# Kernel optimization log

Hardware: AMD Instinct MI355X
Metric: run time of the kernel (lower is better)

## Reference

```python
import jax, jax.numpy as jnp
import numpy as np

H = 16  # num_heads
EPS = 1e-5


def _ln(x, g, b):
    m = x.mean(-1, keepdims=True)
    v = x.var(-1, keepdims=True)
    return (x - m) / jnp.sqrt(v + EPS) * g + b


def _heads(x):
    b, s, d = x.shape
    return x.reshape(b, s, H, d // H).transpose(0, 2, 1, 3)  # [B,H,S,dh]


def _merge_buggy(z):
    # replicate torch view([B,H,S,dh] -> [B,S,H*dh]) WITHOUT head transpose
    b, h, s, dh = z.shape
    return z.reshape(b, s, h * dh)


def _attn(q_in, kv_in, resid, wq, bq, wk, bk, wv, bv, g, be, scale_by_seq, apply_triu):
    q = _heads(q_in @ wq + bq)
    k = _heads(kv_in @ wk + bk)
    v = _heads(kv_in @ wv + bv)
    qk = jnp.einsum('bhqd,bhkd->bhqk', q, k)
    qk = jnp.where(jnp.isnan(qk), -jnp.inf, qk)
    if scale_by_seq:
        qk = qk / jnp.sqrt(jnp.asarray(qk.shape[-1], qk.dtype))  # sqrt(seq_len), as in source
    a = jax.nn.softmax(qk, axis=-1)
    a = jnp.where(jnp.isnan(a), 0.0, a)
    v = jnp.where(jnp.isnan(v), 0.0, v)
    if apply_triu:
        s = a.shape[-1]
        a = a * jnp.triu(jnp.ones((s, s), a.dtype))  # post-softmax multiplicative mask
    z = jnp.einsum('bhqk,bhkd->bhqd', a, v)
    z = _merge_buggy(z)
    return _ln(resid + z, g, be)


def setup_inputs() -> dict:
    key = jax.random.key(0)
    ks = jax.random.split(key, 20)
    B, S, D, F = 2, 2048, 1024, 1024
    p = lambda k, sh: (jax.random.normal(k, sh, jnp.float32) * 0.02)
    inp = {
        'encoded': jax.random.normal(ks[0], (B, S, D), jnp.float32),
        'decoded': jax.random.normal(ks[1], (B, S, D), jnp.float32),
        'sa_wq': p(ks[2], (D, D)), 'sa_bq': jnp.zeros((D,), jnp.float32),
        'sa_wk': p(ks[3], (D, D)), 'sa_bk': jnp.zeros((D,), jnp.float32),
        'sa_wv': p(ks[4], (D, D)), 'sa_bv': jnp.zeros((D,), jnp.float32),
        'sa_g': jnp.ones((D,), jnp.float32), 'sa_b': jnp.zeros((D,), jnp.float32),
        'ca_wq': p(ks[5], (D, D)), 'ca_bq': jnp.zeros((D,), jnp.float32),
        'ca_wk': p(ks[6], (D, D)), 'ca_bk': jnp.zeros((D,), jnp.float32),
        'ca_wv': p(ks[7], (D, D)), 'ca_bv': jnp.zeros((D,), jnp.float32),
        'ca_g': jnp.ones((D,), jnp.float32), 'ca_b': jnp.zeros((D,), jnp.float32),
        'ffn_w1': p(ks[8], (D, F)), 'ffn_b1': jnp.zeros((F,), jnp.float32),
        'ffn_w2': p(ks[9], (F, D)), 'ffn_b2': jnp.zeros((D,), jnp.float32),
        'ffn_g': jnp.ones((D,), jnp.float32), 'ffn_b': jnp.zeros((D,), jnp.float32),
    }
    return inp


def reference(encoded, decoded,
              sa_wq, sa_bq, sa_wk, sa_bk, sa_wv, sa_bv, sa_g, sa_b,
              ca_wq, ca_bq, ca_wk, ca_bk, ca_wv, ca_bv, ca_g, ca_b,
              ffn_w1, ffn_b1, ffn_w2, ffn_b2, ffn_g, ffn_b):
    # masked self-attention (quirky: scale by sqrt(S), post-softmax triu mask)
    x = _attn(decoded, decoded, decoded, sa_wq, sa_bq, sa_wk, sa_bk, sa_wv, sa_bv,
              sa_g, sa_b, scale_by_seq=True, apply_triu=True)
    # cross-attention (no scale, no mask)
    x = _attn(x, encoded, x, ca_wq, ca_bq, ca_wk, ca_bk, ca_wv, ca_bv,
              ca_g, ca_b, scale_by_seq=False, apply_triu=False)
    # FFN with residual + LayerNorm (dropout = identity in eval)
    y = jax.nn.relu(x @ ffn_w1 + ffn_b1) @ ffn_w2 + ffn_b2
    return _ln(y + x, ffn_g, ffn_b)
```

## Files before the change

kernel.cpp:

```cpp
#include <hip/hip_runtime.h>
#include <hip/hip_bf16.h>
#include <cstdint>


typedef __attribute__((ext_vector_type(8))) short bf16x8;
typedef __attribute__((ext_vector_type(4))) float f32x4;
typedef unsigned short u16;

#define MFMA16(a, b, c) __builtin_amdgcn_mfma_f32_16x16x32_bf16((a), (b), (c), 0, 0, 0)

__device__ __forceinline__ u16 f2b(float f) {
    __hip_bfloat16 h = __float2bfloat16(f);
    return __builtin_bit_cast(u16, h);
}
__device__ __forceinline__ float b2f(u16 u) {
    return __builtin_bit_cast(float, (uint32_t)u << 16);
}
__device__ __forceinline__ void g2lds16(const u16* g, u16* l) {
    __builtin_amdgcn_global_load_lds((const __attribute__((address_space(1))) void*)g,
                                     (__attribute__((address_space(3))) void*)l, 16, 0, 0);
}

__global__ __launch_bounds__(256) void cast_bf16_kernel(const float* __restrict__ x,
                                                        u16* __restrict__ y, int n4) {
    int i = blockIdx.x * 256 + threadIdx.x;
    if (i >= n4) return;
    float4 v = reinterpret_cast<const float4*>(x)[i];
    ushort4 o;
    o.x = f2b(v.x); o.y = f2b(v.y); o.z = f2b(v.z); o.w = f2b(v.w);
    reinterpret_cast<ushort4*>(y)[i] = o;
}

__global__ __launch_bounds__(256) void wcast_all_kernel(
    const float* __restrict__ w0, const float* __restrict__ w1,
    const float* __restrict__ w2, const float* __restrict__ w3,
    const float* __restrict__ w4, const float* __restrict__ w5,
    const float* __restrict__ w6, const float* __restrict__ w7,
    u16* __restrict__ wt) {
    __shared__ float t[32][33];
    const float* W;
    switch (blockIdx.z) {
        case 0: W = w0; break; case 1: W = w1; break;
        case 2: W = w2; break; case 3: W = w3; break;
        case 4: W = w4; break; case 5: W = w5; break;
        case 6: W = w6; break; default: W = w7; break;
    }
    u16* Wt = wt + (size_t)blockIdx.z * 1048576;
    int tx = threadIdx.x & 31, ty = threadIdx.x >> 5;
    int bx = blockIdx.x * 32, by = blockIdx.y * 32;
#pragma unroll
    for (int j = 0; j < 4; ++j)
        t[ty + j * 8][tx] = W[(size_t)(by + ty + j * 8) * 1024 + bx + tx];
    __syncthreads();
#pragma unroll
    for (int j = 0; j < 4; ++j)
        Wt[(size_t)(bx + ty + j * 8) * 1024 + by + tx] = f2b(t[tx][ty + j * 8]);
}

__global__ __launch_bounds__(256) void vtrans_kernel(const u16* __restrict__ V,
                                                     u16* __restrict__ Vt) {
    __shared__ u16 t[32][34];
    const int tx = threadIdx.x & 31, ty = threadIdx.x >> 5;
    const int s0 = blockIdx.x * 32, d0 = blockIdx.y * 32, b = blockIdx.z;
    const u16* src = V + (size_t)b * 2048 * 1024;
    u16* dst = Vt + (size_t)b * 1024 * 2048;
#pragma unroll
    for (int j = 0; j < 4; ++j)
        t[ty + j * 8][tx] = src[(size_t)(s0 + ty + j * 8) * 1024 + d0 + tx];
    __syncthreads();
#pragma unroll
    for (int j = 0; j < 4; ++j)
        dst[(size_t)(d0 + ty + j * 8) * 2048 + s0 + tx] = t[tx][ty + j * 8];
}

__global__ __launch_bounds__(256) void gemm_kernel(
    const u16* __restrict__ A0, const u16* __restrict__ A1,
    const u16* __restrict__ Btb,
    const float* __restrict__ bias0, const float* __restrict__ bias1,
    const float* __restrict__ bias2,
    u16* __restrict__ o0, u16* __restrict__ o1, u16* __restrict__ o2,
    int relu, float oscale0) {
    const int K = 1024;
    __shared__ __align__(16) u16 As[2][128][32];
    __shared__ __align__(16) u16 Bs[2][128][32];
    const int tid = threadIdx.x, lane = tid & 63, w = tid >> 6;
    const int wm = w >> 1, wn = w & 1, l15 = lane & 15, l4 = lane >> 4;
    const int nx = gridDim.x;
    const int fhw = blockIdx.y * nx + blockIdx.x;
    const int cpx = (nx * 32) >> 3;
    const int lid = (fhw & 7) * cpx + (fhw >> 3);
    const int bm = (lid & 31) * 128, bn = (lid >> 5) * 128;
    const int which = bn >> 10;
    const u16* A = (which == 0) ? A0 : A1;
    const int srow = lane >> 2, sc = lane & 3;
    const int scs = (sc ^ (srow & 3)) * 8;
    const u16* aW = A + (size_t)(bm + w * 16 + srow) * K + scs;
    const u16* bW = Btb + (size_t)(bn + w * 16 + srow) * K + scs;
    f32x4 acc[4][4] = {};

#define GSTAGE(bf, kt)                                                  \
    do {                                                                \
        g2lds16(aW + (kt), &As[bf][w * 16][0]);                         \
        g2lds16(aW + (size_t)64 * K + (kt), &As[bf][64 + w * 16][0]);   \
        g2lds16(bW + (kt), &Bs[bf][w * 16][0]);                         \
        g2lds16(bW + (size_t)64 * K + (kt), &Bs[bf][64 + w * 16][0]);   \
    } while (0)

    const int nt = K / 32;
    GSTAGE(0, 0);
    for (int t = 0; t < nt; ++t) {
        __syncthreads();
        if (t + 1 < nt) GSTAGE((t + 1) & 1, (t + 1) * 32);
        const int bf = t & 1;
        bf16x8 af[4], bfr[4];
#pragma unroll
        for (int m = 0; m < 4; ++m) {
            int row = wm * 64 + m * 16 + l15;
            af[m] = *reinterpret_cast<const bf16x8*>(&As[bf][row][(l4 ^ (l15 & 3)) * 8]);
        }
#pragma unroll
        for (int n = 0; n < 4; ++n) {
            int row = wn * 64 + n * 16 + l15;
            bfr[n] = *reinterpret_cast<const bf16x8*>(&Bs[bf][row][(l4 ^ (l15 & 3)) * 8]);
        }
        __builtin_amdgcn_s_setprio(1);
#pragma unroll
        for (int m = 0; m < 4; ++m)
#pragma unroll
            for (int n = 0; n < 4; ++n)
                acc[m][n] = MFMA16(af[m], bfr[n], acc[m][n]);
        __builtin_amdgcn_s_setprio(0);
    }
#undef GSTAGE
    const float* bias = which == 0 ? bias0 : (which == 1 ? bias1 : bias2);
    u16* outp = which == 0 ? o0 : (which == 1 ? o1 : o2);
    const float osc = which == 0 ? oscale0 : 1.0f;
    const int bnl = bn & 1023;
#pragma unroll
    for (int m = 0; m < 4; ++m) {
#pragma unroll
        for (int n = 0; n < 4; ++n) {
            int col = bnl + wn * 64 + n * 16 + l15;
            float bv = bias[col];
            int row0 = bm + wm * 64 + m * 16 + l4 * 4;
#pragma unroll
            for (int r = 0; r < 4; ++r) {
                float v = (acc[m][n][r] + bv) * osc;
                if (relu) v = fmaxf(v, 0.f);
                outp[(size_t)(row0 + r) * 1024 + col] = f2b(v);
            }
        }
    }
}

__global__ __launch_bounds__(256) void gemm64_kernel(
    const u16* __restrict__ A, const u16* __restrict__ Btb,
    const float* __restrict__ bias, u16* __restrict__ outp, int relu) {
    const int K = 1024;
    __shared__ __align__(16) u16 As[2][64][32];
    __shared__ __align__(16) u16 Bs[2][128][32];
    const int tid = threadIdx.x, lane = tid & 63, w = tid >> 6;
    const int wm = w >> 1, wn = w & 1, l15 = lane & 15, l4 = lane >> 4;
    const int fhw = blockIdx.y * 8 + blockIdx.x;
    const int lid = (fhw & 7) * 64 + (fhw >> 3);
    const int bm = (lid & 63) * 64, bn = (lid >> 6) * 128;
    const int srow = lane >> 2, sc = lane & 3;
    const int scs = (sc ^ (srow & 3)) * 8;
    const u16* aW = A + (size_t)(bm + w * 16 + srow) * K + scs;
    const u16* bW = Btb + (size_t)(bn + w * 16 + srow) * K + scs;
    f32x4 acc[2][4] = {};

#define GSTAGE64(bf, kt)                                                \
    do {                                                                \
        g2lds16(aW + (kt), &As[bf][w * 16][0]);                         \
        g2lds16(bW + (kt), &Bs[bf][w * 16][0]);                         \
        g2lds16(bW + (size_t)64 * K + (kt), &Bs[bf][64 + w * 16][0]);   \
    } while (0)

    const int nt = K / 32;
    GSTAGE64(0, 0);
    for (int t = 0; t < nt; ++t) {
        __syncthreads();
        if (t + 1 < nt) GSTAGE64((t + 1) & 1, (t + 1) * 32);
        const int bf = t & 1;
        bf16x8 af[2], bfr[4];
#pragma unroll
        for (int m = 0; m < 2; ++m) {
            int row = wm * 32 + m * 16 + l15;
            af[m] = *reinterpret_cast<const bf16x8*>(&As[bf][row][(l4 ^ (l15 & 3)) * 8]);
        }
#pragma unroll
        for (int n = 0; n < 4; ++n) {
            int row = wn * 64 + n * 16 + l15;
            bfr[n] = *reinterpret_cast<const bf16x8*>(&Bs[bf][row][(l4 ^ (l15 & 3)) * 8]);
        }
        __builtin_amdgcn_s_setprio(1);
#pragma unroll
        for (int m = 0; m < 2; ++m)
#pragma unroll
            for (int n = 0; n < 4; ++n)
                acc[m][n] = MFMA16(af[m], bfr[n], acc[m][n]);
        __builtin_amdgcn_s_setprio(0);
    }
#undef GSTAGE64
#pragma unroll
    for (int m = 0; m < 2; ++m) {
#pragma unroll
        for (int n = 0; n < 4; ++n) {
            int col = bn + wn * 64 + n * 16 + l15;
            float bv = bias[col];
            int row0 = bm + wm * 32 + m * 16 + l4 * 4;
#pragma unroll
            for (int r = 0; r < 4; ++r) {
                float v = acc[m][n][r] + bv;
                if (relu) v = fmaxf(v, 0.f);
                outp[(size_t)(row0 + r) * 1024 + col] = f2b(v);
            }
        }
    }
}

template <int CAUSAL>
__global__ __launch_bounds__(256) void attn_kernel(const u16* __restrict__ Qb,
                                                   const u16* __restrict__ Kb,
                                                   const u16* __restrict__ Vt,
                                                   u16* __restrict__ Z) {
    const int S = 2048, D = 1024;
    __shared__ __align__(16) u16 Ks[2][64][64];
    __shared__ __align__(16) u16 Vs[2][64][64];
    __shared__ __align__(16) u16 Ps[4][16][64];
    const int tid = threadIdx.x, lane = tid & 63, w = tid >> 6;
    const int l15 = lane & 15, l4 = lane >> 4;
    const int hwid = blockIdx.x;
    const int wkid = (hwid & 7) * 128 + (hwid >> 3);
    const int qb = wkid & 31, h = (wkid >> 5) & 15, b = wkid >> 9;
    const int q0 = qb * 64 + w * 16;
    const int qg = q0 + l15;
    const size_t baseQ = (size_t)b * S * D + h * 64;
    const size_t baseVt = ((size_t)(b * 16 + h) * 64) * 2048;

    bf16x8 aq0, aq1;
    {
        const u16* qp = Qb + baseQ + (size_t)qg * D + l4 * 8;
        aq0 = *reinterpret_cast<const bf16x8*>(qp);
        aq1 = *reinterpret_cast<const bf16x8*>(qp + 32);
    }
    float lrp0 = 0.f, lrp1 = 0.f, lrp2 = 0.f, lrp3 = 0.f;
    f32x4 Oacc[4] = {};

    const int swzA = (l4 ^ (l15 & 7)) * 8;
    const int swzB = ((l4 + 4) ^ (l15 & 7)) * 8;
    const u16* ksbA = &Ks[0][l15][swzA];
    const u16* ksbB = &Ks[0][l15][swzB];
    const u16* vsbA = &Vs[0][l15][swzA];
    const u16* vsbB = &Vs[0][l15][swzB];
    const int px = l15 & 7;
    u16* pswp[4];
#pragma unroll
    for (int kg = 0; kg < 4; ++kg)
        pswp[kg] = &Ps[w][l15][((2 * kg + (l4 >> 1)) ^ px) * 8 + (l4 & 1) * 4];
    const u16* psrp0 = &Ps[w][l15][((4 * 0 + l4) ^ px) * 8];
    const u16* psrp1 = &Ps[w][l15][((4 * 1 + l4) ^ px) * 8];

    const int srow = lane >> 3, sc8 = lane & 7;
    const int scs = (sc8 ^ srow) * 8;
    const u16* kWn0 = Kb + baseQ + (size_t)(srow + (w * 2 + 0) * 8) * D + scs;
    const u16* kWn1 = Kb + baseQ + (size_t)(srow + (w * 2 + 1) * 8) * D + scs;
    const u16* vWn0 = Vt + baseVt + (size_t)(srow + (w * 2 + 0) * 8) * 2048 + scs;
    const u16* vWn1 = Vt + baseVt + (size_t)(srow + (w * 2 + 1) * 8) * 2048 + scs;

    const int NT = S / 64;
    const int t0pv = CAUSAL ? qb : 0;

    g2lds16(kWn0, &Ks[0][(w * 2 + 0) * 8][0]);
    g2lds16(kWn1, &Ks[0][(w * 2 + 1) * 8][0]);
    kWn0 += 64 * D; kWn1 += 64 * D;
    if (0 >= t0pv) {
        g2lds16(vWn0, &Vs[0][(w * 2 + 0) * 8][0]);
        g2lds16(vWn1, &Vs[0][(w * 2 + 1) * 8][0]);
    }
    vWn0 += 64; vWn1 += 64;

    int tcur = 0;
#define ATILE(B)                                                               \
    do {                                                                       \
        __syncthreads();                                                       \
        if (tcur + 1 < NT) {                                                   \
            g2lds16(kWn0, &Ks[(B) ^ 1][(w * 2 + 0) * 8][0]);                   \
            g2lds16(kWn1, &Ks[(B) ^ 1][(w * 2 + 1) * 8][0]);                   \
            if (tcur + 1 >= t0pv) {                                            \
                g2lds16(vWn0, &Vs[(B) ^ 1][(w * 2 + 0) * 8][0]);               \
                g2lds16(vWn1, &Vs[(B) ^ 1][(w * 2 + 1) * 8][0]);               \
            }                                                                  \
        }                                                                      \
        kWn0 += 64 * D; kWn1 += 64 * D; vWn0 += 64; vWn1 += 64;                \
        const bool dopv = (tcur >= t0pv);                                      \
        const bool maskT = CAUSAL && (tcur == qb);                             \
        bf16x8 vf[2][4];                                                       \
        if (dopv) {                                                            \
            _Pragma("unroll")                                                  \
            for (int n = 0; n < 4; ++n) {                                      \
                vf[0][n] = *reinterpret_cast<const bf16x8*>(                   \
                    vsbA + (B) * 4096 + n * 1024);                             \
                vf[1][n] = *reinterpret_cast<const bf16x8*>(                   \
                    vsbB + (B) * 4096 + n * 1024);                             \
            }                                                                  \
        }                                                                      \
        const f32x4 zero = {0.f, 0.f, 0.f, 0.f};                               \
        _Pragma("unroll")                                                      \
        for (int kg = 0; kg < 4; ++kg) {                                       \
            bf16x8 k0 = *reinterpret_cast<const bf16x8*>(                      \
                ksbA + (B) * 4096 + kg * 1024);                                \
            bf16x8 k1 = *reinterpret_cast<const bf16x8*>(                      \
                ksbB + (B) * 4096 + kg * 1024);                                \
            f32x4 sv = MFMA16(k0, aq0, zero);                                  \
            sv = MFMA16(k1, aq1, sv);                                          \
            float e0 = __builtin_exp2f(sv[0]);                                 \
            float e1 = __builtin_exp2f(sv[1]);                                 \
            float e2 = __builtin_exp2f(sv[2]);                                 \
            float e3 = __builtin_exp2f(sv[3]);                                 \
            lrp0 += e0; lrp1 += e1; lrp2 += e2; lrp3 += e3;                    \
            if (dopv) {                                                        \
                if (maskT) {                                                   \
                    int key = tcur * 64 + kg * 16 + l4 * 4;                    \
                    if (key + 0 < qg) e0 = 0.f;                                \
                    if (key + 1 < qg) e1 = 0.f;                                \
                    if (key + 2 < qg) e2 = 0.f;                                \
                    if (key + 3 < qg) e3 = 0.f;                                \
                }                                                              \
                ushort4 pw;                                                    \
                pw.x = f2b(e0); pw.y = f2b(e1);                                \
                pw.z = f2b(e2); pw.w = f2b(e3);                                \
                *reinterpret_cast<ushort4*>(pswp[kg]) = pw;                    \
            }                                                                  \
        }                                                                      \
        if (dopv) {                                                            \
            asm volatile("s_waitcnt lgkmcnt(0)" ::: "memory");                 \
            __builtin_amdgcn_sched_barrier(0);                                 \
            __builtin_amdgcn_s_setprio(1);                                     \
            bf16x8 pa0 = *reinterpret_cast<const bf16x8*>(psrp0);              \
            bf16x8 pa1 = *reinterpret_cast<const bf16x8*>(psrp1);              \
            _Pragma("unroll")                                                  \
            for (int n = 0; n < 4; ++n)                                        \
                Oacc[n] = MFMA16(vf[0][n], pa0, Oacc[n]);                      \
            _Pragma("unroll")                                                  \
            for (int n = 0; n < 4; ++n)                                        \
                Oacc[n] = MFMA16(vf[1][n], pa1, Oacc[n]);                      \
            __builtin_amdgcn_s_setprio(0);                                     \
        }                                                                      \
        ++tcur;                                                                \
    } while (0)

    for (int i = 0; i < NT / 2; ++i) {
        ATILE(0);
        ATILE(1);
    }
#undef ATILE

    float lr = (lrp0 + lrp1) + (lrp2 + lrp3);
    lr += __shfl_xor(lr, 16);
    lr += __shfl_xor(lr, 32);

    {
        float inv = 1.f / lr;
        int orow = h * 128 + (qg >> 4);
        int oc0 = (qg & 15) * 64;
#pragma unroll
        for (int n = 0; n < 4; ++n) {
            ushort4 o;
            o.x = f2b(Oacc[n][0] * inv); o.y = f2b(Oacc[n][1] * inv);
            o.z = f2b(Oacc[n][2] * inv); o.w = f2b(Oacc[n][3] * inv);
            *reinterpret_cast<ushort4*>(
                &Z[(size_t)b * S * D + (size_t)orow * D + oc0 + n * 16 + l4 * 4]) = o;
        }
    }
}

__global__ __launch_bounds__(256) void add_ln_kernel(const float* __restrict__ resid,
                                                     const u16* __restrict__ zb,
                                                     const float* __restrict__ g,
                                                     const float* __restrict__ bb,
                                                     float* __restrict__ outF,
                                                     u16* __restrict__ outH) {
    const int row = blockIdx.x * 4 + (threadIdx.x >> 6);
    const int lane = threadIdx.x & 63;
    const float* rp = resid + (size_t)row * 1024;
    const u16* zp = zb + (size_t)row * 1024;
    float v[16];
    float s = 0.f, s2 = 0.f;
#pragma unroll
    for (int k = 0; k < 4; ++k) {
        int col = k * 256 + lane * 4;
        float4 rv = *reinterpret_cast<const float4*>(rp + col);
        ushort4 zv = *reinterpret_cast<const ushort4*>(zp + col);
        float x0 = rv.x + b2f(zv.x);
        float x1 = rv.y + b2f(zv.y);
        float x2 = rv.z + b2f(zv.z);
        float x3 = rv.w + b2f(zv.w);
        v[k * 4 + 0] = x0; v[k * 4 + 1] = x1; v[k * 4 + 2] = x2; v[k * 4 + 3] = x3;
        s += x0 + x1 + x2 + x3;
        s2 += x0 * x0 + x1 * x1 + x2 * x2 + x3 * x3;
    }
#pragma unroll
    for (int o = 32; o >= 1; o >>= 1) {
        s += __shfl_xor(s, o);
        s2 += __shfl_xor(s2, o);
    }
    float mean = s * (1.f / 1024.f);
    float var = s2 * (1.f / 1024.f) - mean * mean;
    float rstd = rsqrtf(var + 1e-5f);
#pragma unroll
    for (int k = 0; k < 4; ++k) {
        int col = k * 256 + lane * 4;
        float4 gv = *reinterpret_cast<const float4*>(g + col);
        float4 bv = *reinterpret_cast<const float4*>(bb + col);
        float o0 = (v[k * 4 + 0] - mean) * rstd * gv.x + bv.x;
        float o1 = (v[k * 4 + 1] - mean) * rstd * gv.y + bv.y;
        float o2 = (v[k * 4 + 2] - mean) * rstd * gv.z + bv.z;
        float o3 = (v[k * 4 + 3] - mean) * rstd * gv.w + bv.w;
        if (outF) {
            float4 o = make_float4(o0, o1, o2, o3);
            *reinterpret_cast<float4*>(outF + (size_t)row * 1024 + col) = o;
        }
        if (outH) {
            ushort4 o;
            o.x = f2b(o0); o.y = f2b(o1); o.z = f2b(o2); o.w = f2b(o3);
            *reinterpret_cast<ushort4*>(outH + (size_t)row * 1024 + col) = o;
        }
    }
}

extern "C" void kernel_launch(void* const* d_in, const int* in_sizes, int n_in,
                              void* d_out, int out_size, void* d_ws, size_t ws_size,
                              hipStream_t stream) {
    const float* enc   = (const float*)d_in[0];
    const float* dec   = (const float*)d_in[1];
    const float* sa_wq = (const float*)d_in[2];  const float* sa_bq = (const float*)d_in[3];
    const float* sa_wk = (const float*)d_in[4];  const float* sa_bk = (const float*)d_in[5];
    const float* sa_wv = (const float*)d_in[6];  const float* sa_bv = (const float*)d_in[7];
    const float* sa_g  = (const float*)d_in[8];  const float* sa_b  = (const float*)d_in[9];
    const float* ca_wq = (const float*)d_in[10]; const float* ca_bq = (const float*)d_in[11];
    const float* ca_wk = (const float*)d_in[12]; const float* ca_bk = (const float*)d_in[13];
    const float* ca_wv = (const float*)d_in[14]; const float* ca_bv = (const float*)d_in[15];
    const float* ca_g  = (const float*)d_in[16]; const float* ca_b  = (const float*)d_in[17];
    const float* w1    = (const float*)d_in[18]; const float* b1    = (const float*)d_in[19];
    const float* w2    = (const float*)d_in[20]; const float* b2    = (const float*)d_in[21];
    const float* fg    = (const float*)d_in[22]; const float* fb    = (const float*)d_in[23];
    float* out = (float*)d_out;

    const size_t WSZ = 1048576;
    const size_t ASZ = 4194304;

    u16* wt   = (u16*)d_ws;
    u16* decB = wt + 8 * WSZ;
    u16* encB = decB + ASZ;
    u16* qB   = encB + ASZ;
    u16* kB   = qB + ASZ;
    u16* vB   = kB + ASZ;
    u16* zB   = vB + ASZ;
    float* x1f = (float*)(zB + ASZ);
    u16* xb   = (u16*)(x1f + ASZ);

    const float Q_SCALE_SELF = 0.031879354f;
    const float Q_SCALE_CROSS = 1.4426950408889634f;

    wcast_all_kernel<<<dim3(32, 32, 8), 256, 0, stream>>>(sa_wq, sa_wk, sa_wv, ca_wq,
                                                          ca_wk, ca_wv, w1, w2, wt);
    cast_bf16_kernel<<<4096, 256, 0, stream>>>(dec, decB, (int)(ASZ / 4));
    cast_bf16_kernel<<<4096, 256, 0, stream>>>(enc, encB, (int)(ASZ / 4));

    gemm_kernel<<<dim3(24, 32), 256, 0, stream>>>(decB, decB, wt,
                                                  sa_bq, sa_bk, sa_bv, qB, kB, vB,
                                                  0, Q_SCALE_SELF);
    vtrans_kernel<<<dim3(64, 32, 2), 256, 0, stream>>>(vB, xb);
    attn_kernel<1><<<1024, 256, 0, stream>>>(qB, kB, xb, zB);
    add_ln_kernel<<<1024, 256, 0, stream>>>(dec, zB, sa_g, sa_b, x1f, xb);

    gemm_kernel<<<dim3(24, 32), 256, 0, stream>>>(xb, encB, wt + 3 * WSZ,
                                                  ca_bq, ca_bk, ca_bv, qB, kB, vB,
                                                  0, Q_SCALE_CROSS);
    vtrans_kernel<<<dim3(64, 32, 2), 256, 0, stream>>>(vB, xb);
    attn_kernel<0><<<1024, 256, 0, stream>>>(qB, kB, xb, zB);
    add_ln_kernel<<<1024, 256, 0, stream>>>(x1f, zB, ca_g, ca_b, x1f, xb);

    gemm64_kernel<<<dim3(8, 64), 256, 0, stream>>>(xb, wt + 6 * WSZ, b1, qB, 1);
    gemm64_kernel<<<dim3(8, 64), 256, 0, stream>>>(qB, wt + 7 * WSZ, b2, zB, 0);
    add_ln_kernel<<<1024, 256, 0, stream>>>(x1f, zB, fg, fb, out, nullptr);
}
```

Baseline: 330.8 us.

## Triple-buffer attention K/V tiles with 32-key steps and vmcnt-based waits

The attention kernel now walks keys in 32-wide tiles with a three-stage LDS ring for K and V. It waits on vmcnt counts plus a raw s_barrier instead of a full __syncthreads, so loads two tiles ahead can stay in flight while the current tile is computed. The LDS footprint shrinks and the loop is fully unrolled over 64 tiles. In exchange, each tile carries more barrier overhead relative to its compute. V is now loaded for every tile, including causal tiles that get skipped, and the padded P buffer drops its swizzle, which may bring bank conflicts.

```diff
diff --git a/kernel.cpp b/kernel.cpp
--- a/kernel.cpp
+++ b/kernel.cpp
@@ -226,9 +226,9 @@
                                                    const u16* __restrict__ Vt,
                                                    u16* __restrict__ Z) {
     const int S = 2048, D = 1024;
-    __shared__ __align__(16) u16 Ks[2][64][64];
-    __shared__ __align__(16) u16 Vs[2][64][64];
-    __shared__ __align__(16) u16 Ps[4][16][64];
+    __shared__ __align__(16) u16 Ks[3][32][64];
+    __shared__ __align__(16) u16 Vs[3][64][32];
+    __shared__ __align__(16) u16 Ps[4][16][40];
     const int tid = threadIdx.x, lane = tid & 63, w = tid >> 6;
     const int l15 = lane & 15, l4 = lane >> 4;
     const int hwid = blockIdx.x;
@@ -248,71 +248,52 @@
     float lrp0 = 0.f, lrp1 = 0.f, lrp2 = 0.f, lrp3 = 0.f;
     f32x4 Oacc[4] = {};
 
-    const int swzA = (l4 ^ (l15 & 7)) * 8;
-    const int swzB = ((l4 + 4) ^ (l15 & 7)) * 8;
-    const u16* ksbA = &Ks[0][l15][swzA];
-    const u16* ksbB = &Ks[0][l15][swzB];
-    const u16* vsbA = &Vs[0][l15][swzA];
-    const u16* vsbB = &Vs[0][l15][swzB];
-    const int px = l15 & 7;
-    u16* pswp[4];
-#pragma unroll
-    for (int kg = 0; kg < 4; ++kg)
-        pswp[kg] = &Ps[w][l15][((2 * kg + (l4 >> 1)) ^ px) * 8 + (l4 & 1) * 4];
-    const u16* psrp0 = &Ps[w][l15][((4 * 0 + l4) ^ px) * 8];
-    const u16* psrp1 = &Ps[w][l15][((4 * 1 + l4) ^ px) * 8];
-
-    const int srow = lane >> 3, sc8 = lane & 7;
-    const int scs = (sc8 ^ srow) * 8;
-    const u16* kWn0 = Kb + baseQ + (size_t)(srow + (w * 2 + 0) * 8) * D + scs;
-    const u16* kWn1 = Kb + baseQ + (size_t)(srow + (w * 2 + 1) * 8) * D + scs;
-    const u16* vWn0 = Vt + baseVt + (size_t)(srow + (w * 2 + 0) * 8) * 2048 + scs;
-    const u16* vWn1 = Vt + baseVt + (size_t)(srow + (w * 2 + 1) * 8) * 2048 + scs;
-
-    const int NT = S / 64;
-    const int t0pv = CAUSAL ? qb : 0;
-
-    g2lds16(kWn0, &Ks[0][(w * 2 + 0) * 8][0]);
-    g2lds16(kWn1, &Ks[0][(w * 2 + 1) * 8][0]);
-    kWn0 += 64 * D; kWn1 += 64 * D;
-    if (0 >= t0pv) {
-        g2lds16(vWn0, &Vs[0][(w * 2 + 0) * 8][0]);
-        g2lds16(vWn1, &Vs[0][(w * 2 + 1) * 8][0]);
-    }
-    vWn0 += 64; vWn1 += 64;
+    const u16* ksbA = &Ks[0][l15][(l4 ^ (l15 & 7)) * 8];
+    const u16* ksbB = &Ks[0][l15][((l4 + 4) ^ (l15 & 7)) * 8];
+    const u16* vsb  = &Vs[0][l15][(l4 ^ (l15 & 3)) * 8];
+    u16* pswb = &Ps[w][l15][l4 * 4];
+    const u16* psrb = &Ps[w][l15][l4 * 8];
+
+    const u16* kWn = Kb + baseQ + (size_t)(w * 8 + (lane >> 3)) * D +
+                     ((lane & 7) ^ (lane >> 3)) * 8;
+    const u16* vWn = Vt + baseVt + (size_t)(w * 16 + (lane >> 2)) * 2048 +
+                     (((lane & 3) ^ ((lane >> 2) & 3)) * 8);
+
+    const int t0pv = CAUSAL ? (2 * qb) : 0;
+
+    g2lds16(kWn, &Ks[0][w * 8][0]);
+    g2lds16(vWn, &Vs[0][w * 16][0]);
+    kWn += 32 * D; vWn += 32;
+    g2lds16(kWn, &Ks[1][w * 8][0]);
+    g2lds16(vWn, &Vs[1][w * 16][0]);
+    kWn += 32 * D; vWn += 32;
 
     int tcur = 0;
-#define ATILE(B)                                                               \
+#define ATILE(B, VCSTR, DOSTAGE)                                               \
     do {                                                                       \
-        __syncthreads();                                                       \
-        if (tcur + 1 < NT) {                                                   \
-            g2lds16(kWn0, &Ks[(B) ^ 1][(w * 2 + 0) * 8][0]);                   \
-            g2lds16(kWn1, &Ks[(B) ^ 1][(w * 2 + 1) * 8][0]);                   \
-            if (tcur + 1 >= t0pv) {                                            \
-                g2lds16(vWn0, &Vs[(B) ^ 1][(w * 2 + 0) * 8][0]);               \
-                g2lds16(vWn1, &Vs[(B) ^ 1][(w * 2 + 1) * 8][0]);               \
-            }                                                                  \
+        asm volatile("s_waitcnt " VCSTR ::: "memory");                         \
+        __builtin_amdgcn_s_barrier();                                          \
+        if (DOSTAGE) {                                                         \
+            g2lds16(kWn, &Ks[((B) + 2) % 3][w * 8][0]);                        \
+            g2lds16(vWn, &Vs[((B) + 2) % 3][w * 16][0]);                       \
         }                                                                      \
-        kWn0 += 64 * D; kWn1 += 64 * D; vWn0 += 64; vWn1 += 64;                \
-        const bool dopv = (tcur >= t0pv);                                      \
-        const bool maskT = CAUSAL && (tcur == qb);                             \
-        bf16x8 vf[2][4];                                                       \
+        kWn += 32 * D; vWn += 32;                                              \
+        const bool dopv = (!CAUSAL) || (tcur >= t0pv);                         \
+        const bool maskT = CAUSAL && dopv && (tcur * 32 < q0 + 16);            \
+        bf16x8 vf[4];                                                          \
         if (dopv) {                                                            \
             _Pragma("unroll")                                                  \
-            for (int n = 0; n < 4; ++n) {                                      \
-                vf[0][n] = *reinterpret_cast<const bf16x8*>(                   \
-                    vsbA + (B) * 4096 + n * 1024);                             \
-                vf[1][n] = *reinterpret_cast<const bf16x8*>(                   \
-                    vsbB + (B) * 4096 + n * 1024);                             \
-            }                                                                  \
+            for (int n = 0; n < 4; ++n)                                        \
+                vf[n] = *reinterpret_cast<const bf16x8*>(                      \
+                    vsb + (B) * 2048 + n * 512);                               \
         }                                                                      \
         const f32x4 zero = {0.f, 0.f, 0.f, 0.f};                               \
         _Pragma("unroll")                                                      \
-        for (int kg = 0; kg < 4; ++kg) {                                       \
+        for (int kg = 0; kg < 2; ++kg) {                                       \
             bf16x8 k0 = *reinterpret_cast<const bf16x8*>(                      \
-                ksbA + (B) * 4096 + kg * 1024);                                \
+                ksbA + (B) * 2048 + kg * 1024);                                \
             bf16x8 k1 = *reinterpret_cast<const bf16x8*>(                      \
-                ksbB + (B) * 4096 + kg * 1024);                                \
+                ksbB + (B) * 2048 + kg * 1024);                                \
             f32x4 sv = MFMA16(k0, aq0, zero);                                  \
             sv = MFMA16(k1, aq1, sv);                                          \
             float e0 = __builtin_exp2f(sv[0]);                                 \
@@ -322,7 +303,7 @@
             lrp0 += e0; lrp1 += e1; lrp2 += e2; lrp3 += e3;                    \
             if (dopv) {                                                        \
                 if (maskT) {                                                   \
-                    int key = tcur * 64 + kg * 16 + l4 * 4;                    \
+                    int key = tcur * 32 + kg * 16 + l4 * 4;                    \
                     if (key + 0 < qg) e0 = 0.f;                                \
                     if (key + 1 < qg) e1 = 0.f;                                \
                     if (key + 2 < qg) e2 = 0.f;                                \
@@ -331,30 +312,31 @@
                 ushort4 pw;                                                    \
                 pw.x = f2b(e0); pw.y = f2b(e1);                                \
                 pw.z = f2b(e2); pw.w = f2b(e3);                                \
-                *reinterpret_cast<ushort4*>(pswp[kg]) = pw;                    \
+                *reinterpret_cast<ushort4*>(pswb + kg * 16) = pw;              \
             }                                                                  \
         }                                                                      \
         if (dopv) {                                                            \
             asm volatile("s_waitcnt lgkmcnt(0)" ::: "memory");                 \
             __builtin_amdgcn_sched_barrier(0);                                 \
+            bf16x8 pa = *reinterpret_cast<const bf16x8*>(psrb);                \
             __builtin_amdgcn_s_setprio(1);                                     \
-            bf16x8 pa0 = *reinterpret_cast<const bf16x8*>(psrp0);              \
-            bf16x8 pa1 = *reinterpret_cast<const bf16x8*>(psrp1);              \
             _Pragma("unroll")                                                  \
             for (int n = 0; n < 4; ++n)                                        \
-                Oacc[n] = MFMA16(vf[0][n], pa0, Oacc[n]);                      \
-            _Pragma("unroll")                                                  \
-            for (int n = 0; n < 4; ++n)                                        \
-                Oacc[n] = MFMA16(vf[1][n], pa1, Oacc[n]);                      \
+                Oacc[n] = MFMA16(vf[n], pa, Oacc[n]);                          \
             __builtin_amdgcn_s_setprio(0);                                     \
         }                                                                      \
         ++tcur;                                                                \
     } while (0)
 
-    for (int i = 0; i < NT / 2; ++i) {
-        ATILE(0);
-        ATILE(1);
-    }
+    for (int i = 0; i < 20; ++i) {
+        ATILE(0, "vmcnt(2)", true);
+        ATILE(1, "vmcnt(2)", true);
+        ATILE(2, "vmcnt(2)", true);
+    }
+    ATILE(0, "vmcnt(2)", true);
+    ATILE(1, "vmcnt(2)", true);
+    ATILE(2, "vmcnt(2)", false);
+    ATILE(0, "vmcnt(0)", false);
 #undef ATILE
 
     float lr = (lrp0 + lrp1) + (lrp2 + lrp3);
```

Measured after the change: 343.7 us. 3.9% more time.

## Double attention query tile to 128 rows with 8 waves sharing K/V tiles

Applied to the files above, without the earlier changes.

Each attention workgroup now covers 128 query rows with 8 waves (512 threads) instead of 64 rows with 4 waves. Every K/V tile loaded into LDS is reused by twice as many queries, which halves global K/V traffic, and each wave issues one async LDS copy per tile instead of two. The causal path computes a per-wave diagonal tile so the PV skip and masking stay correct. In exchange there are half as many workgroups, larger barriers over 8 waves, and a coarser causal imbalance, where the first four waves of a block do extra V loads they may not need.

```diff
diff --git a/kernel.cpp b/kernel.cpp
--- a/kernel.cpp
+++ b/kernel.cpp
@@ -221,20 +221,20 @@
 }
 
 template <int CAUSAL>
-__global__ __launch_bounds__(256) void attn_kernel(const u16* __restrict__ Qb,
-                                                   const u16* __restrict__ Kb,
-                                                   const u16* __restrict__ Vt,
-                                                   u16* __restrict__ Z) {
+__global__ __launch_bounds__(512, 6) void attn_kernel(const u16* __restrict__ Qb,
+                                                      const u16* __restrict__ Kb,
+                                                      const u16* __restrict__ Vt,
+                                                      u16* __restrict__ Z) {
     const int S = 2048, D = 1024;
     __shared__ __align__(16) u16 Ks[2][64][64];
     __shared__ __align__(16) u16 Vs[2][64][64];
-    __shared__ __align__(16) u16 Ps[4][16][64];
+    __shared__ __align__(16) u16 Ps[8][16][64];
     const int tid = threadIdx.x, lane = tid & 63, w = tid >> 6;
     const int l15 = lane & 15, l4 = lane >> 4;
     const int hwid = blockIdx.x;
-    const int wkid = (hwid & 7) * 128 + (hwid >> 3);
-    const int qb = wkid & 31, h = (wkid >> 5) & 15, b = wkid >> 9;
-    const int q0 = qb * 64 + w * 16;
+    const int wkid = (hwid & 7) * 64 + (hwid >> 3);
+    const int qb = wkid & 15, h = (wkid >> 4) & 15, b = wkid >> 8;
+    const int q0 = qb * 128 + w * 16;
     const int qg = q0 + l15;
     const size_t baseQ = (size_t)b * S * D + h * 64;
     const size_t baseVt = ((size_t)(b * 16 + h) * 64) * 2048;
@@ -262,40 +262,31 @@
     const u16* psrp0 = &Ps[w][l15][((4 * 0 + l4) ^ px) * 8];
     const u16* psrp1 = &Ps[w][l15][((4 * 1 + l4) ^ px) * 8];
 
-    const int srow = lane >> 3, sc8 = lane & 7;
-    const int scs = (sc8 ^ srow) * 8;
-    const u16* kWn0 = Kb + baseQ + (size_t)(srow + (w * 2 + 0) * 8) * D + scs;
-    const u16* kWn1 = Kb + baseQ + (size_t)(srow + (w * 2 + 1) * 8) * D + scs;
-    const u16* vWn0 = Vt + baseVt + (size_t)(srow + (w * 2 + 0) * 8) * 2048 + scs;
-    const u16* vWn1 = Vt + baseVt + (size_t)(srow + (w * 2 + 1) * 8) * 2048 + scs;
+    const int srw = lane >> 3, sc8 = lane & 7;
+    const int scs = (sc8 ^ srw) * 8;
+    const u16* kWn = Kb + baseQ + (size_t)(w * 8 + srw) * D + scs;
+    const u16* vWn = Vt + baseVt + (size_t)(w * 8 + srw) * 2048 + scs;
 
     const int NT = S / 64;
-    const int t0pv = CAUSAL ? qb : 0;
-
-    g2lds16(kWn0, &Ks[0][(w * 2 + 0) * 8][0]);
-    g2lds16(kWn1, &Ks[0][(w * 2 + 1) * 8][0]);
-    kWn0 += 64 * D; kWn1 += 64 * D;
-    if (0 >= t0pv) {
-        g2lds16(vWn0, &Vs[0][(w * 2 + 0) * 8][0]);
-        g2lds16(vWn1, &Vs[0][(w * 2 + 1) * 8][0]);
-    }
-    vWn0 += 64; vWn1 += 64;
+    const int t0blk = CAUSAL ? (2 * qb) : 0;
+    const int dtile = CAUSAL ? (2 * qb + (w >> 2)) : 0;
+
+    g2lds16(kWn, &Ks[0][w * 8][0]);
+    kWn += 64 * D;
+    if (0 >= t0blk) g2lds16(vWn, &Vs[0][w * 8][0]);
+    vWn += 64;
 
     int tcur = 0;
 #define ATILE(B)                                                               \
     do {                                                                       \
         __syncthreads();                                                       \
         if (tcur + 1 < NT) {                                                   \
-            g2lds16(kWn0, &Ks[(B) ^ 1][(w * 2 + 0) * 8][0]);                   \
-            g2lds16(kWn1, &Ks[(B) ^ 1][(w * 2 + 1) * 8][0]);                   \
-            if (tcur + 1 >= t0pv) {                                            \
-                g2lds16(vWn0, &Vs[(B) ^ 1][(w * 2 + 0) * 8][0]);               \
-                g2lds16(vWn1, &Vs[(B) ^ 1][(w * 2 + 1) * 8][0]);               \
-            }                                                                  \
+            g2lds16(kWn, &Ks[(B) ^ 1][w * 8][0]);                              \
+            if (tcur + 1 >= t0blk) g2lds16(vWn, &Vs[(B) ^ 1][w * 8][0]);       \
         }                                                                      \
-        kWn0 += 64 * D; kWn1 += 64 * D; vWn0 += 64; vWn1 += 64;                \
-        const bool dopv = (tcur >= t0pv);                                      \
-        const bool maskT = CAUSAL && (tcur == qb);                             \
+        kWn += 64 * D; vWn += 64;                                              \
+        const bool dopv = (!CAUSAL) || (tcur >= dtile);                        \
+        const bool maskT = CAUSAL && (tcur == dtile);                          \
         bf16x8 vf[2][4];                                                       \
         if (dopv) {                                                            \
             _Pragma("unroll")                                                  \
@@ -473,14 +464,14 @@
                                                   sa_bq, sa_bk, sa_bv, qB, kB, vB,
                                                   0, Q_SCALE_SELF);
     vtrans_kernel<<<dim3(64, 32, 2), 256, 0, stream>>>(vB, xb);
-    attn_kernel<1><<<1024, 256, 0, stream>>>(qB, kB, xb, zB);
+    attn_kernel<1><<<512, 512, 0, stream>>>(qB, kB, xb, zB);
     add_ln_kernel<<<1024, 256, 0, stream>>>(dec, zB, sa_g, sa_b, x1f, xb);
 
     gemm_kernel<<<dim3(24, 32), 256, 0, stream>>>(xb, encB, wt + 3 * WSZ,
                                                   ca_bq, ca_bk, ca_bv, qB, kB, vB,
                                                   0, Q_SCALE_CROSS);
     vtrans_kernel<<<dim3(64, 32, 2), 256, 0, stream>>>(vB, xb);
-    attn_kernel<0><<<1024, 256, 0, stream>>>(qB, kB, xb, zB);
+    attn_kernel<0><<<512, 512, 0, stream>>>(qB, kB, xb, zB);
     add_ln_kernel<<<1024, 256, 0, stream>>>(x1f, zB, ca_g, ca_b, x1f, xb);
 
     gemm64_kernel<<<dim3(8, 64), 256, 0, stream>>>(xb, wt + 6 * WSZ, b1, qB, 1);
```

Measured after the change: 801.2 us. 142% more time.

## Overlap cross-attention K/V projection GEMM with masked self-attention in one kernel

Applied to the files above, without the earlier changes.

Adds a combined kernel whose blocks either run the causal self-attention tiles or compute the cross-attention K/V projection of the encoder, splitting the block ids roughly 2:1 between the two roles. The cross-attention K/V GEMM no longer depends on the self-attention result, so it runs concurrently and fills idle compute left by the triangular self-attention work. The later cross-attention GEMM then computes only Q. K is written into the decB buffer, and V into vB is later transposed. This adds shared-memory and register pressure from both code paths in one kernel. The ordering relies on decB not being needed after the casts.

```diff
diff --git a/kernel.cpp b/kernel.cpp
--- a/kernel.cpp
+++ b/kernel.cpp
@@ -360,7 +360,6 @@
     float lr = (lrp0 + lrp1) + (lrp2 + lrp3);
     lr += __shfl_xor(lr, 16);
     lr += __shfl_xor(lr, 32);
-
     {
         float inv = 1.f / lr;
         int orow = h * 128 + (qg >> 4);
@@ -372,6 +371,234 @@
             o.z = f2b(Oacc[n][2] * inv); o.w = f2b(Oacc[n][3] * inv);
             *reinterpret_cast<ushort4*>(
                 &Z[(size_t)b * S * D + (size_t)orow * D + oc0 + n * 16 + l4 * 4]) = o;
+        }
+    }
+}
+
+__global__ __launch_bounds__(256) void fat_kernel(
+    const u16* __restrict__ Qb, const u16* __restrict__ Kb,
+    const u16* __restrict__ Vt, u16* __restrict__ Z,
+    const u16* __restrict__ Aenc, const u16* __restrict__ Btb,
+    const float* __restrict__ biasK, const float* __restrict__ biasV,
+    u16* __restrict__ oK, u16* __restrict__ oV) {
+    __shared__ __align__(16) u16 smem[20480];
+    const int tid = threadIdx.x, lane = tid & 63, w = tid >> 6;
+    const int bid = blockIdx.x;
+    const int xcd = bid & 7, lid2 = bid >> 3;
+    const int rrr = lid2 % 3;
+    const int l15 = lane & 15, l4 = lane >> 4;
+
+    if (rrr != 2) {
+        const int S = 2048, D = 1024;
+        u16* KsB = smem;
+        u16* VsB = smem + 8192;
+        u16* PsB = smem + 16384;
+        const int wkid = xcd * 128 + ((lid2 / 3) * 2 + rrr);
+        const int qb = wkid & 31, h = (wkid >> 5) & 15, b = wkid >> 9;
+        const int q0 = qb * 64 + w * 16;
+        const int qg = q0 + l15;
+        const size_t baseQ = (size_t)b * S * D + h * 64;
+        const size_t baseVt = ((size_t)(b * 16 + h) * 64) * 2048;
+
+        bf16x8 aq0, aq1;
+        {
+            const u16* qp = Qb + baseQ + (size_t)qg * D + l4 * 8;
+            aq0 = *reinterpret_cast<const bf16x8*>(qp);
+            aq1 = *reinterpret_cast<const bf16x8*>(qp + 32);
+        }
+        float lrp0 = 0.f, lrp1 = 0.f, lrp2 = 0.f, lrp3 = 0.f;
+        f32x4 Oacc[4] = {};
+
+        const int swzA = (l4 ^ (l15 & 7)) * 8;
+        const int swzB = ((l4 + 4) ^ (l15 & 7)) * 8;
+        const u16* ksbA = KsB + l15 * 64 + swzA;
+        const u16* ksbB = KsB + l15 * 64 + swzB;
+        const u16* vsbA = VsB + l15 * 64 + swzA;
+        const u16* vsbB = VsB + l15 * 64 + swzB;
+        const int px = l15 & 7;
+        u16* pswp[4];
+#pragma unroll
+        for (int kg = 0; kg < 4; ++kg)
+            pswp[kg] = PsB + w * 1024 + l15 * 64 +
+                       ((2 * kg + (l4 >> 1)) ^ px) * 8 + (l4 & 1) * 4;
+        const u16* psrp0 = PsB + w * 1024 + l15 * 64 + ((0 + l4) ^ px) * 8;
+        const u16* psrp1 = PsB + w * 1024 + l15 * 64 + ((4 + l4) ^ px) * 8;
+
+        const int srow = lane >> 3, sc8 = lane & 7;
+        const int scs = (sc8 ^ srow) * 8;
+        const u16* kWn0 = Kb + baseQ + (size_t)(srow + (w * 2 + 0) * 8) * D + scs;
+        const u16* kWn1 = Kb + baseQ + (size_t)(srow + (w * 2 + 1) * 8) * D + scs;
+        const u16* vWn0 = Vt + baseVt + (size_t)(srow + (w * 2 + 0) * 8) * 2048 + scs;
+        const u16* vWn1 = Vt + baseVt + (size_t)(srow + (w * 2 + 1) * 8) * 2048 + scs;
+
+        const int NT = S / 64;
+        const int t0pv = qb;
+
+        g2lds16(kWn0, KsB + (w * 2 + 0) * 512);
+        g2lds16(kWn1, KsB + (w * 2 + 1) * 512);
+        kWn0 += 64 * D; kWn1 += 64 * D;
+        if (0 >= t0pv) {
+            g2lds16(vWn0, VsB + (w * 2 + 0) * 512);
+            g2lds16(vWn1, VsB + (w * 2 + 1) * 512);
+        }
+        vWn0 += 64; vWn1 += 64;
+
+        int tcur = 0;
+#define FTILE(B)                                                               \
+    do {                                                                       \
+        __syncthreads();                                                       \
+        if (tcur + 1 < NT) {                                                   \
+            g2lds16(kWn0, KsB + ((B) ^ 1) * 4096 + (w * 2 + 0) * 512);         \
+            g2lds16(kWn1, KsB + ((B) ^ 1) * 4096 + (w * 2 + 1) * 512);         \
+            if (tcur + 1 >= t0pv) {                                            \
+                g2lds16(vWn0, VsB + ((B) ^ 1) * 4096 + (w * 2 + 0) * 512);     \
+                g2lds16(vWn1, VsB + ((B) ^ 1) * 4096 + (w * 2 + 1) * 512);     \
+            }                                                                  \
+        }                                                                      \
+        kWn0 += 64 * D; kWn1 += 64 * D; vWn0 += 64; vWn1 += 64;                \
+        const bool dopv = (tcur >= t0pv);                                      \
+        const bool maskT = (tcur == qb);                                       \
+        bf16x8 vf[2][4];                                                       \
+        if (dopv) {                                                            \
+            _Pragma("unroll")                                                  \
+            for (int n = 0; n < 4; ++n) {                                      \
+                vf[0][n] = *reinterpret_cast<const bf16x8*>(                   \
+                    vsbA + (B) * 4096 + n * 1024);                             \
+                vf[1][n] = *reinterpret_cast<const bf16x8*>(                   \
+                    vsbB + (B) * 4096 + n * 1024);                             \
+            }                                                                  \
+        }                                                                      \
+        const f32x4 zero = {0.f, 0.f, 0.f, 0.f};                               \
+        _Pragma("unroll")                                                      \
+        for (int kg = 0; kg < 4; ++kg) {                                       \
+            bf16x8 k0 = *reinterpret_cast<const bf16x8*>(                      \
+                ksbA + (B) * 4096 + kg * 1024);                                \
+            bf16x8 k1 = *reinterpret_cast<const bf16x8*>(                      \
+                ksbB + (B) * 4096 + kg * 1024);                                \
+            f32x4 sv = MFMA16(k0, aq0, zero);                                  \
+            sv = MFMA16(k1, aq1, sv);                                          \
+            float e0 = __builtin_exp2f(sv[0]);                                 \
+            float e1 = __builtin_exp2f(sv[1]);                                 \
+            float e2 = __builtin_exp2f(sv[2]);                                 \
+            float e3 = __builtin_exp2f(sv[3]);                                 \
+            lrp0 += e0; lrp1 += e1; lrp2 += e2; lrp3 += e3;                    \
+            if (dopv) {                                                        \
+                if (maskT) {                                                   \
+                    int key = tcur * 64 + kg * 16 + l4 * 4;                    \
+                    if (key + 0 < qg) e0 = 0.f;                                \
+                    if (key + 1 < qg) e1 = 0.f;                                \
+                    if (key + 2 < qg) e2 = 0.f;                                \
+                    if (key + 3 < qg) e3 = 0.f;                                \
+                }                                                              \
+                ushort4 pw;                                                    \
+                pw.x = f2b(e0); pw.y = f2b(e1);                                \
+                pw.z = f2b(e2); pw.w = f2b(e3);                                \
+                *reinterpret_cast<ushort4*>(pswp[kg]) = pw;                    \
+            }                                                                  \
+        }                                                                      \
+        if (dopv) {                                                            \
+            asm volatile("s_waitcnt lgkmcnt(0)" ::: "memory");                 \
+            __builtin_amdgcn_sched_barrier(0);                                 \
+            __builtin_amdgcn_s_setprio(1);                                     \
+            bf16x8 pa0 = *reinterpret_cast<const bf16x8*>(psrp0);              \
+            bf16x8 pa1 = *reinterpret_cast<const bf16x8*>(psrp1);              \
+            _Pragma("unroll")                                                  \
+            for (int n = 0; n < 4; ++n)                                        \
+                Oacc[n] = MFMA16(vf[0][n], pa0, Oacc[n]);                      \
+            _Pragma("unroll")                                                  \
+            for (int n = 0; n < 4; ++n)                                        \
+                Oacc[n] = MFMA16(vf[1][n], pa1, Oacc[n]);                      \
+            __builtin_amdgcn_s_setprio(0);                                     \
+        }                                                                      \
+        ++tcur;                                                                \
+    } while (0)
+
+        for (int i = 0; i < NT / 2; ++i) {
+            FTILE(0);
+            FTILE(1);
+        }
+#undef FTILE
+
+        float lr = (lrp0 + lrp1) + (lrp2 + lrp3);
+        lr += __shfl_xor(lr, 16);
+        lr += __shfl_xor(lr, 32);
+        float inv = 1.f / lr;
+        int orow = h * 128 + (qg >> 4);
+        int oc0 = (qg & 15) * 64;
+#pragma unroll
+        for (int n = 0; n < 4; ++n) {
+            ushort4 o;
+            o.x = f2b(Oacc[n][0] * inv); o.y = f2b(Oacc[n][1] * inv);
+            o.z = f2b(Oacc[n][2] * inv); o.w = f2b(Oacc[n][3] * inv);
+            *reinterpret_cast<ushort4*>(
+                &Z[(size_t)b * S * D + (size_t)orow * D + oc0 + n * 16 + l4 * 4]) = o;
+        }
+    } else {
+        const int K = 1024;
+        u16* AsB = smem;
+        u16* BsB = smem + 8192;
+        const int wm = w >> 1, wn = w & 1;
+        const int lidg = xcd * 64 + lid2 / 3;
+        const int bm = (lidg & 31) * 128, bn = (lidg >> 5) * 128;
+        const int which = bn >> 10;
+        const int srow = lane >> 2, sc = lane & 3;
+        const int scs = (sc ^ (srow & 3)) * 8;
+        const u16* aW = Aenc + (size_t)(bm + w * 16 + srow) * K + scs;
+        const u16* bW = Btb + (size_t)(bn + w * 16 + srow) * K + scs;
+        f32x4 acc[4][4] = {};
+
+#define FGST(bf, kt)                                                           \
+    do {                                                                       \
+        g2lds16(aW + (kt), AsB + (bf) * 4096 + w * 512);                       \
+        g2lds16(aW + (size_t)64 * K + (kt), AsB + (bf) * 4096 + 2048 + w * 512); \
+        g2lds16(bW + (kt), BsB + (bf) * 4096 + w * 512);                       \
+        g2lds16(bW + (size_t)64 * K + (kt), BsB + (bf) * 4096 + 2048 + w * 512); \
+    } while (0)
+
+        const int nt = K / 32;
+        FGST(0, 0);
+        for (int t = 0; t < nt; ++t) {
+            __syncthreads();
+            if (t + 1 < nt) FGST((t + 1) & 1, (t + 1) * 32);
+            const int bf = t & 1;
+            bf16x8 af[4], bfr[4];
+#pragma unroll
+            for (int m = 0; m < 4; ++m) {
+                int row = wm * 64 + m * 16 + l15;
+                af[m] = *reinterpret_cast<const bf16x8*>(
+                    AsB + bf * 4096 + row * 32 + (l4 ^ (l15 & 3)) * 8);
+            }
+#pragma unroll
+            for (int n = 0; n < 4; ++n) {
+                int row = wn * 64 + n * 16 + l15;
+                bfr[n] = *reinterpret_cast<const bf16x8*>(
+                    BsB + bf * 4096 + row * 32 + (l4 ^ (l15 & 3)) * 8);
+            }
+            __builtin_amdgcn_s_setprio(1);
+#pragma unroll
+            for (int m = 0; m < 4; ++m)
+#pragma unroll
+                for (int n = 0; n < 4; ++n)
+                    acc[m][n] = MFMA16(af[m], bfr[n], acc[m][n]);
+            __builtin_amdgcn_s_setprio(0);
+        }
+#undef FGST
+        const float* bias = which == 0 ? biasK : biasV;
+        u16* outp = which == 0 ? oK : oV;
+        const int bnl = bn & 1023;
+#pragma unroll
+        for (int m = 0; m < 4; ++m) {
+#pragma unroll
+            for (int n = 0; n < 4; ++n) {
+                int col = bnl + wn * 64 + n * 16 + l15;
+                float bv = bias[col];
+                int row0 = bm + wm * 64 + m * 16 + l4 * 4;
+#pragma unroll
+                for (int r = 0; r < 4; ++r) {
+                    float v = acc[m][n][r] + bv;
+                    outp[(size_t)(row0 + r) * 1024 + col] = f2b(v);
+                }
+            }
         }
     }
 }
@@ -442,9 +669,9 @@
     const float* ca_wq = (const float*)d_in[10]; const float* ca_bq = (const float*)d_in[11];
     const float* ca_wk = (const float*)d_in[12]; const float* ca_bk = (const float*)d_in[13];
     const float* ca_wv = (const float*)d_in[14]; const float* ca_bv = (const float*)d_in[15];
-    const float* ca_g  = (const float*)d_in[16]; const float* ca_b  = (const float*)d_in[17];
     const float* w1    = (const float*)d_in[18]; const float* b1    = (const float*)d_in[19];
     const float* w2    = (const float*)d_in[20]; const float* b2    = (const float*)d_in[21];
+    const float* ca_g  = (const float*)d_in[16]; const float* ca_b  = (const float*)d_in[17];
     const float* fg    = (const float*)d_in[22]; const float* fb    = (const float*)d_in[23];
     float* out = (float*)d_out;
 
@@ -473,14 +700,17 @@
                                                   sa_bq, sa_bk, sa_bv, qB, kB, vB,
                                                   0, Q_SCALE_SELF);
     vtrans_kernel<<<dim3(64, 32, 2), 256, 0, stream>>>(vB, xb);
-    attn_kernel<1><<<1024, 256, 0, stream>>>(qB, kB, xb, zB);
+
+    fat_kernel<<<1536, 256, 0, stream>>>(qB, kB, xb, zB,
+                                         encB, wt + 4 * WSZ, ca_bk, ca_bv,
+                                         decB, vB);
     add_ln_kernel<<<1024, 256, 0, stream>>>(dec, zB, sa_g, sa_b, x1f, xb);
 
-    gemm_kernel<<<dim3(24, 32), 256, 0, stream>>>(xb, encB, wt + 3 * WSZ,
-                                                  ca_bq, ca_bk, ca_bv, qB, kB, vB,
-                                                  0, Q_SCALE_CROSS);
+    gemm_kernel<<<dim3(8, 32), 256, 0, stream>>>(xb, xb, wt + 3 * WSZ,
+                                                 ca_bq, ca_bq, ca_bq, qB, qB, qB,
+                                                 0, Q_SCALE_CROSS);
     vtrans_kernel<<<dim3(64, 32, 2), 256, 0, stream>>>(vB, xb);
-    attn_kernel<0><<<1024, 256, 0, stream>>>(qB, kB, xb, zB);
+    attn_kernel<0><<<1024, 256, 0, stream>>>(qB, decB, xb, zB);
     add_ln_kernel<<<1024, 256, 0, stream>>>(x1f, zB, ca_g, ca_b, x1f, xb);
 
     gemm64_kernel<<<dim3(8, 64), 256, 0, stream>>>(xb, wt + 6 * WSZ, b1, qB, 1);
```

After: 407.9 us. 1.23x slower.
